# Kernel optimization log

Hardware: AMD Instinct MI355X
Metric: run time of the kernel (lower is better)

## Reference

```python
import jax, jax.numpy as jnp
import numpy as np


def setup_inputs() -> dict:
    key = jax.random.key(0)
    k1, k2 = jax.random.split(key)
    B, Lq, Ls, D = 16, 2048, 2048, 512
    query = jax.random.normal(k1, (B, Lq, D), dtype=jnp.float32)
    support = jax.random.normal(k2, (B, Ls, D), dtype=jnp.float32)
    return {"query": query, "support": support}


def reference(query, support):
    # attn: [B, Lq, Ls] = softmax(query @ support^T, axis=-1)
    logits = jnp.einsum("bqd,bsd->bqs", query, support)
    attn = jax.nn.softmax(logits, axis=-1)
    # attended support: [B, Lq, D]
    attended = jnp.einsum("bqs,bsd->bqd", attn, support)
    # score: [B, Lq] = sum over D of query * attended
    score = jnp.sum(query * attended, axis=-1)
    return score
```

## Files before the change

kernel.cpp:

```cpp
#include <hip/hip_runtime.h>
#include <hip/hip_bf16.h>

#define B_  16
#define LQ  2048
#define LS  2048
#define DD  512
#define BQ  256
#define BS  256
#define BK  64
#define NSB (LS / BS)
#define NKC (DD / BK)
#define NSPLIT 4

static_assert(NKC == 8, "stage>>3 math assumes NKC==8");

typedef short bf16x8 __attribute__((ext_vector_type(8)));
typedef float f32x4  __attribute__((ext_vector_type(4)));

__device__ __forceinline__ void load_lds16(const void* g, void* l) {
  __builtin_amdgcn_global_load_lds((const __attribute__((address_space(1))) void*)g,
                                   (__attribute__((address_space(3))) void*)l,
                                   16, 0, 0);
}

__device__ __forceinline__ unsigned short f2bf(float f) {
  union { float f; unsigned int u; } v; v.f = f;
  unsigned int r = v.u + 0x7fffu + ((v.u >> 16) & 1u);
  return (unsigned short)(r >> 16);
}

__global__ __launch_bounds__(256) void cvt_kernel(const float* __restrict__ Q,
                                                  const float* __restrict__ S,
                                                  unsigned short* __restrict__ Qw,
                                                  unsigned short* __restrict__ Sw,
                                                  int nblk) {
  int blk = blockIdx.x;
  const float* src; unsigned short* dst;
  if (blk < nblk) { src = Q; dst = Qw; } else { src = S; dst = Sw; blk -= nblk; }
  int i = blk * 256 + threadIdx.x;
  float4 f = ((const float4*)src)[i];
  ushort4 u;
  u.x = f2bf(f.x); u.y = f2bf(f.y); u.z = f2bf(f.z); u.w = f2bf(f.w);
  ((ushort4*)dst)[i] = u;
}

__global__ __launch_bounds__(512, 2) void attn_kernel(const unsigned short* __restrict__ Qw,
                                                      const unsigned short* __restrict__ Sw,
                                                      float* __restrict__ out,
                                                      float* __restrict__ pm,
                                                      float* __restrict__ pse,
                                                      float* __restrict__ psel,
                                                      int nsplit) {
  __shared__ __align__(16) unsigned short sQ[2][BQ * BK];
  __shared__ __align__(16) unsigned short sS[2][BS * BK];

  const int pid = blockIdx.x + (blockIdx.y << 3) + (blockIdx.z << 7);
  const int nch = (nsplit << 7) >> 3;
  const int lid = (pid & 7) * nch + (pid >> 3);
  const int qb  = lid & 7;
  const int b   = (lid >> 3) & 15;
  const int spl = lid >> 7;

  const int tid  = threadIdx.x;
  const int w    = tid >> 6;
  const int lane = tid & 63;
  const int h    = w & 1;
  const int g    = w >> 1;
  const int col  = lane & 15;
  const int quad = lane >> 4;
  const int c7   = col & 7;

  const int q0 = qb * BQ;
  const unsigned short* Qb = Qw + (size_t)b * LQ * DD;
  const unsigned short* Sb = Sw + (size_t)b * LS * DD;

  float mst[4] = { -INFINITY, -INFINITY, -INFINITY, -INFINITY };
  float se[4]  = { 0.f, 0.f, 0.f, 0.f };
  float sel[4] = { 0.f, 0.f, 0.f, 0.f };

  f32x4 acc[8][4];
#pragma unroll
  for (int st = 0; st < 8; ++st)
#pragma unroll
    for (int qt = 0; qt < 4; ++qt)
      acc[st][qt] = (f32x4){0.f, 0.f, 0.f, 0.f};

  const int rr = lane >> 3;
  const int cc = ((lane & 7) ^ rr) * 8;

  const int sbs = spl * (NSB / nsplit);
  const int nst = (NSB / nsplit) * NKC;

  auto issue_stage = [&](int t_i, int buf) {
    const int kc = t_i & 7;
    if (w < 4) {
      const unsigned short* gp = Qb + (size_t)(q0 + w * 64 + rr) * DD + kc * BK + cc;
      unsigned short* lp = &sQ[buf][(w * 64) * BK];
#pragma unroll
      for (int i = 0; i < 8; ++i)
        load_lds16(gp + (size_t)i * 8 * DD, lp + i * 8 * BK);
    } else {
      const int sb = sbs + (t_i >> 3);
      const unsigned short* gp = Sb + (size_t)(sb * BS + (w - 4) * 64 + rr) * DD + kc * BK + cc;
      unsigned short* lp = &sS[buf][((w - 4) * 64) * BK];
#pragma unroll
      for (int i = 0; i < 8; ++i)
        load_lds16(gp + (size_t)i * 8 * DD, lp + i * 8 * BK);
    }
  };

  issue_stage(0, 0);
  asm volatile("s_waitcnt vmcnt(0)" ::: "memory");
  __builtin_amdgcn_s_barrier();
  int cur = 0;

#pragma unroll 1
  for (int t = 0; t < nst; ++t) {
    const int tn = t + 1;
    const unsigned short* bq = &sQ[cur][0];
    const unsigned short* bs = &sS[cur][0];

    bf16x8 aq[4], asv[4];
#pragma unroll
    for (int p = 0; p < 4; ++p) {
      const int kk = p >> 1, sh = p & 1;
      const int koff = ((kk * 4 + quad) ^ c7) * 8;
      if (p == 0 && tn < nst) issue_stage(tn, cur ^ 1);
      if (sh == 0) {
#pragma unroll
        for (int qt = 0; qt < 4; ++qt)
          aq[qt] = *(const bf16x8*)&bq[(g * 64 + qt * 16 + col) * BK + koff];
      }
#pragma unroll
      for (int st = 0; st < 4; ++st)
        asv[st] = *(const bf16x8*)&bs[(h * 128 + (sh * 4 + st) * 16 + col) * BK + koff];
      __builtin_amdgcn_s_barrier();
      asm volatile("s_waitcnt lgkmcnt(0)" ::: "memory");
      __builtin_amdgcn_sched_barrier(0);
      __builtin_amdgcn_s_setprio(1);
#pragma unroll
      for (int qt = 0; qt < 4; ++qt)
#pragma unroll
        for (int st = 0; st < 4; ++st)
          acc[sh * 4 + st][qt] = __builtin_amdgcn_mfma_f32_16x16x32_bf16(asv[st], aq[qt], acc[sh * 4 + st][qt], 0, 0, 0);
      __builtin_amdgcn_s_setprio(0);
      if (p == 3)
        asm volatile("s_waitcnt vmcnt(0)" ::: "memory");
      __builtin_amdgcn_s_barrier();
    }
    cur ^= 1;

    if ((t & (NKC - 1)) == NKC - 1) {
#pragma unroll
      for (int qt = 0; qt < 4; ++qt) {
        float lmax = mst[qt];
#pragma unroll
        for (int st = 0; st < 8; ++st)
#pragma unroll
          for (int r = 0; r < 4; ++r)
            lmax = fmaxf(lmax, acc[st][qt][r]);
        lmax = fmaxf(lmax, __shfl_xor(lmax, 16, 64));
        lmax = fmaxf(lmax, __shfl_xor(lmax, 32, 64));
        float alpha = __expf(mst[qt] - lmax);
        float pe = 0.f, pel = 0.f;
#pragma unroll
        for (int st = 0; st < 8; ++st)
#pragma unroll
          for (int r = 0; r < 4; ++r) {
            float l = acc[st][qt][r];
            float e = __expf(l - lmax);
            pe += e;
            pel = fmaf(e, l, pel);
          }
        pe  += __shfl_xor(pe, 16, 64);  pe  += __shfl_xor(pe, 32, 64);
        pel += __shfl_xor(pel, 16, 64); pel += __shfl_xor(pel, 32, 64);
        se[qt]  = fmaf(se[qt],  alpha, pe);
        sel[qt] = fmaf(sel[qt], alpha, pel);
        mst[qt] = lmax;
#pragma unroll
        for (int st = 0; st < 8; ++st)
          acc[st][qt] = (f32x4){0.f, 0.f, 0.f, 0.f};
      }
    }
  }

  __syncthreads();
  float* red = (float*)&sQ[0][0];
  if (quad == 0) {
#pragma unroll
    for (int qt = 0; qt < 4; ++qt) {
      int qq = g * 64 + qt * 16 + col;
      red[h * 256 + qq]        = mst[qt];
      red[512 + h * 256 + qq]  = se[qt];
      red[1024 + h * 256 + qq] = sel[qt];
    }
  }
  __syncthreads();
  if (h == 0 && quad == 0) {
#pragma unroll
    for (int qt = 0; qt < 4; ++qt) {
      int qq = g * 64 + qt * 16 + col;
      float m0 = red[qq],       m1 = red[256 + qq];
      float M  = fmaxf(m0, m1);
      float a0 = __expf(m0 - M), a1 = __expf(m1 - M);
      float SE  = red[512 + qq]  * a0 + red[512 + 256 + qq]  * a1;
      float SEL = red[1024 + qq] * a0 + red[1024 + 256 + qq] * a1;
      size_t qi = (size_t)b * LQ + q0 + qq;
      if (nsplit == 1) {
        out[qi] = SEL / SE;
      } else {
        pm[qi * NSPLIT + spl]   = M;
        pse[qi * NSPLIT + spl]  = SE;
        psel[qi * NSPLIT + spl] = SEL;
      }
    }
  }
}

__global__ __launch_bounds__(256) void combine_kernel(const float* __restrict__ pm,
                                                      const float* __restrict__ pse,
                                                      const float* __restrict__ psel,
                                                      float* __restrict__ out) {
  int i = blockIdx.x * blockDim.x + threadIdx.x;
  if (i >= B_ * LQ) return;
  float M = -INFINITY;
#pragma unroll
  for (int s = 0; s < NSPLIT; ++s) M = fmaxf(M, pm[i * NSPLIT + s]);
  float SE = 0.f, SEL = 0.f;
#pragma unroll
  for (int s = 0; s < NSPLIT; ++s) {
    float a = __expf(pm[i * NSPLIT + s] - M);
    SE  = fmaf(pse[i * NSPLIT + s],  a, SE);
    SEL = fmaf(psel[i * NSPLIT + s], a, SEL);
  }
  out[i] = SEL / SE;
}

__global__ __launch_bounds__(256) void fallback_kernel(const float* __restrict__ Q,
                                                       const float* __restrict__ S,
                                                       float* __restrict__ out) {
  __shared__ float qv[DD];
  __shared__ float red[256];
  const int b = blockIdx.y, qi = blockIdx.x, tid = threadIdx.x;
  const float* qrow = Q + ((size_t)b * LQ + qi) * DD;
  for (int d = tid; d < DD; d += 256) qv[d] = qrow[d];
  __syncthreads();
  const float* Sb = S + (size_t)b * LS * DD;
  float m = -INFINITY, se = 0.f, sel = 0.f;
  for (int s = tid; s < LS; s += 256) {
    const float* srow = Sb + (size_t)s * DD;
    float dot = 0.f;
    for (int d = 0; d < DD; ++d) dot = fmaf(qv[d], srow[d], dot);
    float mn = fmaxf(m, dot);
    float a = __expf(m - mn);
    float e = __expf(dot - mn);
    se  = se * a + e;
    sel = sel * a + e * dot;
    m = mn;
  }
  red[tid] = m; __syncthreads();
  for (int o = 128; o > 0; o >>= 1) { if (tid < o) red[tid] = fmaxf(red[tid], red[tid + o]); __syncthreads(); }
  float M = red[0]; __syncthreads();
  float a = __expf(m - M); se *= a; sel *= a;
  red[tid] = se; __syncthreads();
  for (int o = 128; o > 0; o >>= 1) { if (tid < o) red[tid] += red[tid + o]; __syncthreads(); }
  float SE = red[0]; __syncthreads();
  red[tid] = sel; __syncthreads();
  for (int o = 128; o > 0; o >>= 1) { if (tid < o) red[tid] += red[tid + o]; __syncthreads(); }
  float SEL = red[0];
  if (tid == 0) out[(size_t)b * LQ + qi] = SEL / SE;
}

extern "C" void kernel_launch(void* const* d_in, const int* in_sizes, int n_in,
                              void* d_out, int out_size, void* d_ws, size_t ws_size,
                              hipStream_t stream) {
  const float* Q = (const float*)d_in[0];
  const float* S = (const float*)d_in[1];
  float* out = (float*)d_out;
  const size_t nelem = (size_t)B_ * LQ * DD;
  const size_t need_base  = 2 * nelem * sizeof(unsigned short);
  const size_t part_elems = (size_t)B_ * LQ * NSPLIT;
  const size_t need_split = need_base + 3 * part_elems * sizeof(float);

  if (ws_size >= need_base) {
    unsigned short* Qw = (unsigned short*)d_ws;
    unsigned short* Sw = Qw + nelem;
    int nblk = (int)(nelem / 4 / 256);
    cvt_kernel<<<2 * nblk, 256, 0, stream>>>(Q, S, Qw, Sw, nblk);
    if (ws_size >= need_split) {
      float* pm   = (float*)(Sw + nelem);
      float* pse  = pm + part_elems;
      float* psel = pse + part_elems;
      attn_kernel<<<dim3(LQ / BQ, B_, NSPLIT), 512, 0, stream>>>(Qw, Sw, out, pm, pse, psel, NSPLIT);
      combine_kernel<<<(B_ * LQ + 255) / 256, 256, 0, stream>>>(pm, pse, psel, out);
    } else {
      attn_kernel<<<dim3(LQ / BQ, B_, 1), 512, 0, stream>>>(Qw, Sw, out, nullptr, nullptr, nullptr, 1);
    }
  } else {
    fallback_kernel<<<dim3(LQ, B_), 256, 0, stream>>>(Q, S, out);
  }
}
```

Baseline: 222.9 us.

## Shrink attention tiles to 128x128 with 256-thread blocks and simpler pipeline

Halves the Q and S tile sizes to 128 and the block size to 256 threads, giving four times as many workgroups. All four waves now load both Q and S slices, and the main loop uses a single wait-and-barrier prefetch point per stage instead of four phased barriers with priority hints. This is meant to raise occupancy and cut barrier overhead. In exchange, each tile gets less data reuse, so global and LDS traffic per FLOP doubles.

```diff
diff --git a/kernel.cpp b/kernel.cpp
--- a/kernel.cpp
+++ b/kernel.cpp
@@ -5,8 +5,8 @@
 #define LQ  2048
 #define LS  2048
 #define DD  512
-#define BQ  256
-#define BS  256
+#define BQ  128
+#define BS  128
 #define BK  64
 #define NSB (LS / BS)
 #define NKC (DD / BK)
@@ -44,7 +44,7 @@
   ((ushort4*)dst)[i] = u;
 }
 
-__global__ __launch_bounds__(512, 2) void attn_kernel(const unsigned short* __restrict__ Qw,
+__global__ __launch_bounds__(256, 2) void attn_kernel(const unsigned short* __restrict__ Qw,
                                                       const unsigned short* __restrict__ Sw,
                                                       float* __restrict__ out,
                                                       float* __restrict__ pm,
@@ -54,12 +54,12 @@
   __shared__ __align__(16) unsigned short sQ[2][BQ * BK];
   __shared__ __align__(16) unsigned short sS[2][BS * BK];
 
-  const int pid = blockIdx.x + (blockIdx.y << 3) + (blockIdx.z << 7);
-  const int nch = (nsplit << 7) >> 3;
+  const int pid = blockIdx.x + (blockIdx.y << 4) + (blockIdx.z << 8);
+  const int nch = (nsplit << 8) >> 3;
   const int lid = (pid & 7) * nch + (pid >> 3);
-  const int qb  = lid & 7;
-  const int b   = (lid >> 3) & 15;
-  const int spl = lid >> 7;
+  const int qb  = lid & 15;
+  const int b   = (lid >> 4) & 15;
+  const int spl = lid >> 8;
 
   const int tid  = threadIdx.x;
   const int w    = tid >> 6;
@@ -78,9 +78,9 @@
   float se[4]  = { 0.f, 0.f, 0.f, 0.f };
   float sel[4] = { 0.f, 0.f, 0.f, 0.f };
 
-  f32x4 acc[8][4];
-#pragma unroll
-  for (int st = 0; st < 8; ++st)
+  f32x4 acc[4][4];
+#pragma unroll
+  for (int st = 0; st < 4; ++st)
 #pragma unroll
     for (int qt = 0; qt < 4; ++qt)
       acc[st][qt] = (f32x4){0.f, 0.f, 0.f, 0.f};
@@ -93,20 +93,17 @@
 
   auto issue_stage = [&](int t_i, int buf) {
     const int kc = t_i & 7;
-    if (w < 4) {
-      const unsigned short* gp = Qb + (size_t)(q0 + w * 64 + rr) * DD + kc * BK + cc;
-      unsigned short* lp = &sQ[buf][(w * 64) * BK];
-#pragma unroll
-      for (int i = 0; i < 8; ++i)
-        load_lds16(gp + (size_t)i * 8 * DD, lp + i * 8 * BK);
-    } else {
-      const int sb = sbs + (t_i >> 3);
-      const unsigned short* gp = Sb + (size_t)(sb * BS + (w - 4) * 64 + rr) * DD + kc * BK + cc;
-      unsigned short* lp = &sS[buf][((w - 4) * 64) * BK];
-#pragma unroll
-      for (int i = 0; i < 8; ++i)
-        load_lds16(gp + (size_t)i * 8 * DD, lp + i * 8 * BK);
-    }
+    const int sb = sbs + (t_i >> 3);
+    const unsigned short* gq = Qb + (size_t)(q0 + w * 32 + rr) * DD + kc * BK + cc;
+    const unsigned short* gs = Sb + (size_t)(sb * BS + w * 32 + rr) * DD + kc * BK + cc;
+    unsigned short* lq = &sQ[buf][(w * 32) * BK];
+    unsigned short* ls = &sS[buf][(w * 32) * BK];
+#pragma unroll
+    for (int i = 0; i < 4; ++i)
+      load_lds16(gq + (size_t)i * 8 * DD, lq + i * 8 * BK);
+#pragma unroll
+    for (int i = 0; i < 4; ++i)
+      load_lds16(gs + (size_t)i * 8 * DD, ls + i * 8 * BK);
   };
 
   issue_stage(0, 0);
@@ -117,36 +114,33 @@
 #pragma unroll 1
   for (int t = 0; t < nst; ++t) {
     const int tn = t + 1;
+    asm volatile("s_waitcnt lgkmcnt(0)" ::: "memory");
+    __builtin_amdgcn_s_barrier();
+    if (tn < nst) {
+      issue_stage(tn, cur ^ 1);
+      asm volatile("s_waitcnt vmcnt(8)" ::: "memory");
+    } else {
+      asm volatile("s_waitcnt vmcnt(0)" ::: "memory");
+    }
+    __builtin_amdgcn_s_barrier();
+
     const unsigned short* bq = &sQ[cur][0];
     const unsigned short* bs = &sS[cur][0];
-
-    bf16x8 aq[4], asv[4];
-#pragma unroll
-    for (int p = 0; p < 4; ++p) {
-      const int kk = p >> 1, sh = p & 1;
+#pragma unroll
+    for (int kk = 0; kk < 2; ++kk) {
       const int koff = ((kk * 4 + quad) ^ c7) * 8;
-      if (p == 0 && tn < nst) issue_stage(tn, cur ^ 1);
-      if (sh == 0) {
-#pragma unroll
-        for (int qt = 0; qt < 4; ++qt)
-          aq[qt] = *(const bf16x8*)&bq[(g * 64 + qt * 16 + col) * BK + koff];
-      }
+      bf16x8 asv[4], aq[4];
 #pragma unroll
       for (int st = 0; st < 4; ++st)
-        asv[st] = *(const bf16x8*)&bs[(h * 128 + (sh * 4 + st) * 16 + col) * BK + koff];
-      __builtin_amdgcn_s_barrier();
-      asm volatile("s_waitcnt lgkmcnt(0)" ::: "memory");
-      __builtin_amdgcn_sched_barrier(0);
-      __builtin_amdgcn_s_setprio(1);
+        asv[st] = *(const bf16x8*)&bs[(h * 64 + st * 16 + col) * BK + koff];
 #pragma unroll
       for (int qt = 0; qt < 4; ++qt)
-#pragma unroll
-        for (int st = 0; st < 4; ++st)
-          acc[sh * 4 + st][qt] = __builtin_amdgcn_mfma_f32_16x16x32_bf16(asv[st], aq[qt], acc[sh * 4 + st][qt], 0, 0, 0);
-      __builtin_amdgcn_s_setprio(0);
-      if (p == 3)
-        asm volatile("s_waitcnt vmcnt(0)" ::: "memory");
-      __builtin_amdgcn_s_barrier();
+        aq[qt] = *(const bf16x8*)&bq[(g * 64 + qt * 16 + col) * BK + koff];
+#pragma unroll
+      for (int qt = 0; qt < 4; ++qt)
+#pragma unroll
+        for (int st = 0; st < 4; ++st)
+          acc[st][qt] = __builtin_amdgcn_mfma_f32_16x16x32_bf16(asv[st], aq[qt], acc[st][qt], 0, 0, 0);
     }
     cur ^= 1;
 
@@ -155,7 +149,7 @@
       for (int qt = 0; qt < 4; ++qt) {
         float lmax = mst[qt];
 #pragma unroll
-        for (int st = 0; st < 8; ++st)
+        for (int st = 0; st < 4; ++st)
 #pragma unroll
           for (int r = 0; r < 4; ++r)
             lmax = fmaxf(lmax, acc[st][qt][r]);
@@ -164,7 +158,7 @@
         float alpha = __expf(mst[qt] - lmax);
         float pe = 0.f, pel = 0.f;
 #pragma unroll
-        for (int st = 0; st < 8; ++st)
+        for (int st = 0; st < 4; ++st)
 #pragma unroll
           for (int r = 0; r < 4; ++r) {
             float l = acc[st][qt][r];
@@ -178,7 +172,7 @@
         sel[qt] = fmaf(sel[qt], alpha, pel);
         mst[qt] = lmax;
 #pragma unroll
-        for (int st = 0; st < 8; ++st)
+        for (int st = 0; st < 4; ++st)
           acc[st][qt] = (f32x4){0.f, 0.f, 0.f, 0.f};
       }
     }
@@ -190,9 +184,9 @@
 #pragma unroll
     for (int qt = 0; qt < 4; ++qt) {
       int qq = g * 64 + qt * 16 + col;
-      red[h * 256 + qq]        = mst[qt];
-      red[512 + h * 256 + qq]  = se[qt];
-      red[1024 + h * 256 + qq] = sel[qt];
+      red[h * 128 + qq]       = mst[qt];
+      red[256 + h * 128 + qq] = se[qt];
+      red[512 + h * 128 + qq] = sel[qt];
     }
   }
   __syncthreads();
@@ -200,11 +194,11 @@
 #pragma unroll
     for (int qt = 0; qt < 4; ++qt) {
       int qq = g * 64 + qt * 16 + col;
-      float m0 = red[qq],       m1 = red[256 + qq];
+      float m0 = red[qq],       m1 = red[128 + qq];
       float M  = fmaxf(m0, m1);
       float a0 = __expf(m0 - M), a1 = __expf(m1 - M);
-      float SE  = red[512 + qq]  * a0 + red[512 + 256 + qq]  * a1;
-      float SEL = red[1024 + qq] * a0 + red[1024 + 256 + qq] * a1;
+      float SE  = red[256 + qq] * a0 + red[256 + 128 + qq] * a1;
+      float SEL = red[512 + qq] * a0 + red[512 + 128 + qq] * a1;
       size_t qi = (size_t)b * LQ + q0 + qq;
       if (nsplit == 1) {
         out[qi] = SEL / SE;
@@ -291,10 +285,10 @@
       float* pm   = (float*)(Sw + nelem);
       float* pse  = pm + part_elems;
       float* psel = pse + part_elems;
-      attn_kernel<<<dim3(LQ / BQ, B_, NSPLIT), 512, 0, stream>>>(Qw, Sw, out, pm, pse, psel, NSPLIT);
+      attn_kernel<<<dim3(LQ / BQ, B_, NSPLIT), 256, 0, stream>>>(Qw, Sw, out, pm, pse, psel, NSPLIT);
       combine_kernel<<<(B_ * LQ + 255) / 256, 256, 0, stream>>>(pm, pse, psel, out);
     } else {
-      attn_kernel<<<dim3(LQ / BQ, B_, 1), 512, 0, stream>>>(Qw, Sw, out, nullptr, nullptr, nullptr, 1);
+      attn_kernel<<<dim3(LQ / BQ, B_, 1), 256, 0, stream>>>(Qw, Sw, out, nullptr, nullptr, nullptr, 1);
     }
   } else {
     fallback_kernel<<<dim3(LQ, B_), 256, 0, stream>>>(Q, S, out);
```

Result: slower. 239.8 us (+7.6%).
